# Optimization experiments

Measured on AMD Instinct MI355X. Metric: run time of the kernel, lower is better.

Reference implementation:

```python
import jax, jax.numpy as jnp
import numpy as np

NEG_INF_DIAG = 1000000.0

def setup_inputs() -> dict:
    key = jax.random.key(0)
    k1, k2, k3 = jax.random.split(key, 3)
    B, N, S, D = 64, 32, 256, 128
    return {
        "query_embeddings": jax.random.normal(k1, (B, N, D), dtype=jnp.float32),
        "doc_embeddings": jax.random.normal(k2, (B, S, D), dtype=jnp.float32),
        "neg_doc_embeddings": jax.random.normal(k3, (B, S, D), dtype=jnp.float32),
    }

def _maxsim(q, d):
    # q: (b, n, dim), d: (b, s, dim) -> (b,) sum over n of max over s of q.d
    return jnp.einsum('bnd,bsd->bns', q, d).max(axis=2).sum(axis=1)

def reference(query_embeddings, doc_embeddings, neg_doc_embeddings):
    pos_scores = _maxsim(query_embeddings, doc_embeddings)
    neg_scores = _maxsim(query_embeddings, neg_doc_embeddings)
    loss = jax.nn.softplus(neg_scores - pos_scores).mean()

    # in-batch term: scores[b, c] = MaxSim(query b, doc c)
    scores = jnp.einsum('bnd,csd->bcns', query_embeddings, doc_embeddings).max(axis=3).sum(axis=2)  # (B, B)
    pos = jnp.diagonal(scores)
    B = scores.shape[0]
    neg = (scores - jnp.eye(B, dtype=scores.dtype) * NEG_INF_DIAG).max(axis=1)
    loss = loss + jax.nn.softplus(neg - pos).mean()
    return loss / 2
```

## Files before the change

### kernel.cpp

```cpp
#include <hip/hip_runtime.h>
#include <hip/hip_bf16.h>

#define B_SZ 64

typedef __attribute__((ext_vector_type(8))) short bf16x8;
typedef __attribute__((ext_vector_type(4))) float f32x4;

static __device__ __forceinline__ unsigned short f2bf(float f) {
    __hip_bfloat16 h = __float2bfloat16(f);
    return *reinterpret_cast<unsigned short*>(&h);
}

static __device__ __forceinline__ bf16x8 cvt_frag(const float* __restrict__ src) {
    float4 a = reinterpret_cast<const float4*>(src)[0];
    float4 b = reinterpret_cast<const float4*>(src)[1];
    union { bf16x8 v; unsigned short u[8]; } t;
    t.u[0] = f2bf(a.x); t.u[1] = f2bf(a.y); t.u[2] = f2bf(a.z); t.u[3] = f2bf(a.w);
    t.u[4] = f2bf(b.x); t.u[5] = f2bf(b.y); t.u[6] = f2bf(b.z); t.u[7] = f2bf(b.w);
    return t.v;
}

#define MFMA(A, Bv, C) __builtin_amdgcn_mfma_f32_16x16x32_bf16(A, Bv, C, 0, 0, 0)

__global__ __launch_bounds__(256) void cvt_permute(const float* __restrict__ q,
                                                   const float* __restrict__ dd,
                                                   const float* __restrict__ nd,
                                                   unsigned short* __restrict__ DP,
                                                   unsigned short* __restrict__ QP) {
    const int blk = blockIdx.x, tid = threadIdx.x;
    if (blk < 2048) {
        const int o = blk * 256 + tid;
        const int doc = o >> 12, rem = o & 4095;
        const float* src = ((doc < 64) ? (dd + (size_t)doc * 32768)
                                       : (nd + (size_t)(doc - 64) * 32768)) + rem * 8;
        bf16x8 v = cvt_frag(src);
        const int s = rem >> 4, k8 = rem & 15;
        const int lane = (k8 & 3) * 16 + (s & 15);
        const int idx = doc * 4096 + (s >> 6) * 1024
                      + (k8 >> 2) * 256
                      + ((s >> 4) & 3) * 64 + lane;
        reinterpret_cast<bf16x8*>(DP)[idx] = v;
    } else {
        const int g = (blk - 2048) * 256 + tid;
        const int b = g >> 9, u = g & 511;
        const int ln = u & 63, mt = (u >> 6) & 1, kk = u >> 7;
        const int n  = mt * 16 + (ln & 15);
        const int k0 = kk * 32 + (ln >> 4) * 8;
        reinterpret_cast<bf16x8*>(QP)[g] = cvt_frag(q + (size_t)b * 4096 + n * 128 + k0);
    }
}

__global__ __launch_bounds__(256, 2) void maxsim_kernel(const unsigned short* __restrict__ QP,
                                                        const unsigned short* __restrict__ DP,
                                                        float* __restrict__ scores) {
    const int wg  = blockIdx.x;
    const int tid = threadIdx.x;
    const int wave = tid >> 6, lane = tid & 63;
    const int l15 = lane & 15;

    __shared__ float wred[8][4][4][8];

    const bf16x8* DP8 = reinterpret_cast<const bf16x8*>(DP);
    const bf16x8* QP8 = reinterpret_cast<const bf16x8*>(QP);

    int c, b0, nb, dcc;
    if (wg < 512) {
        const int x = wg & 7, i = wg >> 3;
        c   = x * 8 + (i & 7);
        b0  = (i >> 3) * 8;
        nb  = 8;
        dcc = c;
    } else {
        b0 = wg - 512; c = 64; nb = 1; dcc = 64 + b0;
    }

    bf16x8 Bv[4][4];
    const bf16x8* dsrc = DP8 + (size_t)dcc * 4096 + wave * 1024 + lane;
    #pragma unroll
    for (int kk = 0; kk < 4; ++kk)
        #pragma unroll
        for (int nt = 0; nt < 4; ++nt)
            Bv[kk][nt] = dsrc[kk * 256 + nt * 64];

    #pragma unroll 2
    for (int bi = 0; bi < nb; ++bi) {
        const int b = b0 + bi;
        bf16x8 Af[4][2];
        const bf16x8* qsrc = QP8 + (size_t)b * 512 + lane;
        #pragma unroll
        for (int kk = 0; kk < 4; ++kk) {
            Af[kk][0] = qsrc[kk * 128];
            Af[kk][1] = qsrc[kk * 128 + 64];
        }
        f32x4 acc[2][4] = {};
        #pragma unroll
        for (int kk = 0; kk < 4; ++kk)
            #pragma unroll
            for (int nt = 0; nt < 4; ++nt) {
                acc[0][nt] = MFMA(Af[kk][0], Bv[kk][nt], acc[0][nt]);
                acc[1][nt] = MFMA(Af[kk][1], Bv[kk][nt], acc[1][nt]);
            }
        #pragma unroll
        for (int mt = 0; mt < 2; ++mt)
            #pragma unroll
            for (int r = 0; r < 4; ++r) {
                float m = fmaxf(fmaxf(acc[mt][0][r], acc[mt][1][r]),
                                fmaxf(acc[mt][2][r], acc[mt][3][r]));
                m = fmaxf(m, __shfl_xor(m, 1, 64));
                m = fmaxf(m, __shfl_xor(m, 2, 64));
                m = fmaxf(m, __shfl_xor(m, 4, 64));
                m = fmaxf(m, __shfl_xor(m, 8, 64));
                if (l15 == 0) wred[bi][wave][lane >> 4][mt * 4 + r] = m;
            }
    }
    __syncthreads();

    if (tid < nb * 32) {
        const int bi = tid >> 5, n = tid & 31;
        const int slot = (n >> 4) * 4 + (n & 3);
        const int lhi  = (n >> 2) & 3;
        float m = fmaxf(fmaxf(wred[bi][0][lhi][slot], wred[bi][1][lhi][slot]),
                        fmaxf(wred[bi][2][lhi][slot], wred[bi][3][lhi][slot]));
        m += __shfl_xor(m, 1, 32);
        m += __shfl_xor(m, 2, 32);
        m += __shfl_xor(m, 4, 32);
        m += __shfl_xor(m, 8, 32);
        m += __shfl_xor(m, 16, 32);
        if (n == 0) scores[(size_t)(b0 + bi) * 65 + c] = m;
    }
}

static __device__ __forceinline__ float softplusf(float x) {
    return fmaxf(x, 0.0f) + log1pf(expf(-fabsf(x)));
}

__global__ __launch_bounds__(64) void loss_kernel(const float* __restrict__ scores,
                                                  float* __restrict__ out) {
    const int b = threadIdx.x;
    const float* row = scores + b * 65;
    const float pos  = row[b];
    const float negq = row[64];
    float nib = -1e30f;
    #pragma unroll
    for (int c = 0; c < B_SZ; ++c) {
        float v = row[c] - ((c == b) ? 1000000.0f : 0.0f);
        nib = fmaxf(nib, v);
    }
    float t = softplusf(negq - pos) + softplusf(nib - pos);
    t += __shfl_xor(t, 1, 64);
    t += __shfl_xor(t, 2, 64);
    t += __shfl_xor(t, 4, 64);
    t += __shfl_xor(t, 8, 64);
    t += __shfl_xor(t, 16, 64);
    t += __shfl_xor(t, 32, 64);
    if (b == 0) out[0] = t * (0.5f / 64.0f);
}

extern "C" void kernel_launch(void* const* d_in, const int* in_sizes, int n_in,
                              void* d_out, int out_size, void* d_ws, size_t ws_size,
                              hipStream_t stream) {
    const float* q  = (const float*)d_in[0];
    const float* dd = (const float*)d_in[1];
    const float* nd = (const float*)d_in[2];
    float* out = (float*)d_out;

    unsigned short* DP = (unsigned short*)d_ws;
    unsigned short* QP = DP + (size_t)128 * 32768;
    float* scores = (float*)(QP + (size_t)64 * 4096);

    cvt_permute<<<2176, 256, 0, stream>>>(q, dd, nd, DP, QP);
    maxsim_kernel<<<512 + B_SZ, 256, 0, stream>>>(QP, DP, scores);
    loss_kernel<<<1, 64, 0, stream>>>(scores, out);
}
```

Measured before the change: 92.58 us.

## Fuse bf16 conversion and permutation into maxsim kernel via swizzled LDS staging

```diff
diff --git a/kernel.cpp b/kernel.cpp
--- a/kernel.cpp
+++ b/kernel.cpp
@@ -22,75 +22,69 @@
 
 #define MFMA(A, Bv, C) __builtin_amdgcn_mfma_f32_16x16x32_bf16(A, Bv, C, 0, 0, 0)
 
-__global__ __launch_bounds__(256) void cvt_permute(const float* __restrict__ q,
-                                                   const float* __restrict__ dd,
-                                                   const float* __restrict__ nd,
-                                                   unsigned short* __restrict__ DP,
-                                                   unsigned short* __restrict__ QP) {
-    const int blk = blockIdx.x, tid = threadIdx.x;
-    if (blk < 2048) {
-        const int o = blk * 256 + tid;
-        const int doc = o >> 12, rem = o & 4095;
-        const float* src = ((doc < 64) ? (dd + (size_t)doc * 32768)
-                                       : (nd + (size_t)(doc - 64) * 32768)) + rem * 8;
-        bf16x8 v = cvt_frag(src);
-        const int s = rem >> 4, k8 = rem & 15;
-        const int lane = (k8 & 3) * 16 + (s & 15);
-        const int idx = doc * 4096 + (s >> 6) * 1024
-                      + (k8 >> 2) * 256
-                      + ((s >> 4) & 3) * 64 + lane;
-        reinterpret_cast<bf16x8*>(DP)[idx] = v;
-    } else {
-        const int g = (blk - 2048) * 256 + tid;
-        const int b = g >> 9, u = g & 511;
-        const int ln = u & 63, mt = (u >> 6) & 1, kk = u >> 7;
-        const int n  = mt * 16 + (ln & 15);
-        const int k0 = kk * 32 + (ln >> 4) * 8;
-        reinterpret_cast<bf16x8*>(QP)[g] = cvt_frag(q + (size_t)b * 4096 + n * 128 + k0);
-    }
-}
-
-__global__ __launch_bounds__(256, 2) void maxsim_kernel(const unsigned short* __restrict__ QP,
-                                                        const unsigned short* __restrict__ DP,
-                                                        float* __restrict__ scores) {
+__global__ __launch_bounds__(256, 2) void maxsim_mega(const float* __restrict__ q,
+                                                      const float* __restrict__ dd,
+                                                      const float* __restrict__ nd,
+                                                      float* __restrict__ scores) {
     const int wg  = blockIdx.x;
     const int tid = threadIdx.x;
     const int wave = tid >> 6, lane = tid & 63;
-    const int l15 = lane & 15;
+    const int l15 = lane & 15, lhi = lane >> 4;
 
+    __shared__ bf16x8 docL[4096];
+    __shared__ bf16x8 qL[512];
     __shared__ float wred[8][4][4][8];
 
-    const bf16x8* DP8 = reinterpret_cast<const bf16x8*>(DP);
-    const bf16x8* QP8 = reinterpret_cast<const bf16x8*>(QP);
-
-    int c, b0, nb, dcc;
+    int c, b0, nb;
+    const float* docp;
     if (wg < 512) {
         const int x = wg & 7, i = wg >> 3;
         c   = x * 8 + (i & 7);
         b0  = (i >> 3) * 8;
         nb  = 8;
-        dcc = c;
+        docp = dd + (size_t)c * 32768;
     } else {
-        b0 = wg - 512; c = 64; nb = 1; dcc = 64 + b0;
+        b0 = wg - 512; c = 64; nb = 1;
+        docp = nd + (size_t)b0 * 32768;
     }
 
+    char* lb = reinterpret_cast<char*>(docL);
+    #pragma unroll
+    for (int i = 0; i < 16; ++i) {
+        const int rem_g = i * 256 + tid;
+        bf16x8 v = cvt_frag(docp + (size_t)rem_g * 8);
+        const int ch = rem_g >> 10, rem = rem_g & 1023;
+        const int a = ch * 16384 + ((rem * 16) ^ (((rem >> 4) & 7) << 4));
+        *reinterpret_cast<bf16x8*>(lb + a) = v;
+    }
+    __syncthreads();
+
     bf16x8 Bv[4][4];
-    const bf16x8* dsrc = DP8 + (size_t)dcc * 4096 + wave * 1024 + lane;
     #pragma unroll
     for (int kk = 0; kk < 4; ++kk)
         #pragma unroll
-        for (int nt = 0; nt < 4; ++nt)
-            Bv[kk][nt] = dsrc[kk * 256 + nt * 64];
+        for (int nt = 0; nt < 4; ++nt) {
+            const int rem = (nt * 16 + l15) * 16 + kk * 4 + lhi;
+            const int a = wave * 16384 + ((rem * 16) ^ (((rem >> 4) & 7) << 4));
+            Bv[kk][nt] = *reinterpret_cast<const bf16x8*>(lb + a);
+        }
 
-    #pragma unroll 2
     for (int bi = 0; bi < nb; ++bi) {
         const int b = b0 + bi;
+        #pragma unroll
+        for (int h = 0; h < 2; ++h) {
+            const int g  = h * 256 + tid;
+            const int n  = ((g >> 6) & 1) * 16 + (g & 15);
+            const int k8 = (g >> 7) * 4 + ((g >> 4) & 3);
+            qL[g] = cvt_frag(q + (size_t)b * 4096 + (size_t)(n * 16 + k8) * 8);
+        }
+        __syncthreads();
+
         bf16x8 Af[4][2];
-        const bf16x8* qsrc = QP8 + (size_t)b * 512 + lane;
         #pragma unroll
         for (int kk = 0; kk < 4; ++kk) {
-            Af[kk][0] = qsrc[kk * 128];
-            Af[kk][1] = qsrc[kk * 128 + 64];
+            Af[kk][0] = qL[kk * 128 + lane];
+            Af[kk][1] = qL[kk * 128 + 64 + lane];
         }
         f32x4 acc[2][4] = {};
         #pragma unroll
@@ -110,17 +104,17 @@
                 m = fmaxf(m, __shfl_xor(m, 2, 64));
                 m = fmaxf(m, __shfl_xor(m, 4, 64));
                 m = fmaxf(m, __shfl_xor(m, 8, 64));
-                if (l15 == 0) wred[bi][wave][lane >> 4][mt * 4 + r] = m;
+                if (l15 == 0) wred[bi][wave][lhi][mt * 4 + r] = m;
             }
+        __syncthreads();
     }
-    __syncthreads();
 
     if (tid < nb * 32) {
         const int bi = tid >> 5, n = tid & 31;
         const int slot = (n >> 4) * 4 + (n & 3);
-        const int lhi  = (n >> 2) & 3;
-        float m = fmaxf(fmaxf(wred[bi][0][lhi][slot], wred[bi][1][lhi][slot]),
-                        fmaxf(wred[bi][2][lhi][slot], wred[bi][3][lhi][slot]));
+        const int lh   = (n >> 2) & 3;
+        float m = fmaxf(fmaxf(wred[bi][0][lh][slot], wred[bi][1][lh][slot]),
+                        fmaxf(wred[bi][2][lh][slot], wred[bi][3][lh][slot]));
         m += __shfl_xor(m, 1, 32);
         m += __shfl_xor(m, 2, 32);
         m += __shfl_xor(m, 4, 32);
@@ -164,11 +158,8 @@
     const float* nd = (const float*)d_in[2];
     float* out = (float*)d_out;
 
-    unsigned short* DP = (unsigned short*)d_ws;
-    unsigned short* QP = DP + (size_t)128 * 32768;
-    float* scores = (float*)(QP + (size_t)64 * 4096);
+    float* scores = (float*)d_ws;
 
-    cvt_permute<<<2176, 256, 0, stream>>>(q, dd, nd, DP, QP);
-    maxsim_kernel<<<512 + B_SZ, 256, 0, stream>>>(QP, DP, scores);
+    maxsim_mega<<<512 + B_SZ, 256, 0, stream>>>(q, dd, nd, scores);
     loss_kernel<<<1, 64, 0, stream>>>(scores, out);
 }
```

New measurement: 96.73 us. +4.5%, slower.
